# Performance work log

Measured on AMD Instinct MI355X. Metric: run time of the kernel, lower is better.

## Reference

```python
import jax, jax.numpy as jnp
import numpy as np

D_MODEL = 512
D_STATE = 64
L_SEQ = 4096
BATCH = 4


def _make_A(N):
    # HiPPO-LegS style A: A[n,k] = -sqrt(2n+1)sqrt(2k+1) if n>k, -(n+1) if n==k, 0 else (n,k from 1..N)
    idx = np.arange(1, N + 1, dtype=np.float64)
    M = np.sqrt(2 * idx[:, None] + 1) * np.sqrt(2 * idx[None, :] + 1)
    lower = (idx[:, None] > idx[None, :]).astype(np.float64)
    return -(lower * M + np.diag(idx + 1))


def _discretize(A, B, C, step):
    # bilinear (Tustin) transform
    I = np.eye(A.shape[0])
    BL = np.linalg.inv(I - step / 2.0 * A)
    Ab = BL @ (I + step / 2.0 * A)
    Bb = (BL * step) @ B
    return Ab, Bb, C


def setup_inputs() -> dict:
    key = jax.random.key(0)
    rng = np.random.RandomState(0)
    A = _make_A(D_STATE)
    B = rng.randn(D_STATE, 1)
    C = rng.randn(1, D_STATE)
    Ab, Bb, Cb = _discretize(A, B, C, step=1.0 / L_SEQ)
    u = jax.random.normal(key, (BATCH, L_SEQ, D_MODEL), dtype=jnp.float32)
    return {
        "u": u,
        "A_": jnp.asarray(Ab, dtype=jnp.float32),
        "B_": jnp.asarray(Bb, dtype=jnp.float32),
        "C_": jnp.asarray(Cb, dtype=jnp.float32),
    }


def reference(u, A_, B_, C_):
    # u: (B, L, D) -> flatten channels: (BD, L)
    b, L, d = u.shape
    uc = u.transpose(0, 2, 1).reshape(b * d, L)
    N = A_.shape[0]
    b_vec = B_[:, 0]  # (N,)
    c_vec = C_[0]     # (N,)

    def step(x, u_k):
        # x: (BD, N), u_k: (BD,)
        # x_k = A_ @ x_{k-1}^T + B_ @ u_k^T  (expressed batched as x @ A_.T + outer)
        x_new = x @ A_.T + u_k[:, None] * b_vec[None, :]
        y_k = x_new @ c_vec  # (BD,)
        return x_new, y_k

    x0 = jnp.zeros((b * d, N), dtype=u.dtype)
    _, ys = jax.lax.scan(step, x0, uc.T)  # ys: (L, BD)
    y = ys.T.reshape(b, d, L).transpose(0, 2, 1)  # (B, L, D)
    return y
```

## Files before the change

### kernel.cpp

```cpp
#include <hip/hip_runtime.h>

#define L_SEQ   4096
#define D_MODEL 512
#define NSEQ    2048
#define CH      128
#define NC      32

#define OFF_P    0
#define OFF_W1T  4096
#define OFF_WOUT 12288
#define OFF_KLOC 20480
#define OFF_GX   20736

#define BC(v, j) __int_as_float(__builtin_amdgcn_readlane(__float_as_int(v), (j)))

__global__ __launch_bounds__(256) void k_prep(
    const float* __restrict__ A, const float* __restrict__ B,
    const float* __restrict__ C, float* __restrict__ ws) {
  __shared__ float M0[64][68];
  __shared__ float M1[64][68];
  __shared__ float Asv[64][68];
  __shared__ float vrT[128][65];
  __shared__ float Cs[64], Bsh[64];

  const int tid = threadIdx.x;
  if (tid < 64) { Cs[tid] = C[tid]; Bsh[tid] = B[tid]; }
  for (int e = tid; e < 4096; e += 256) {
    const float a = A[e];
    M0[e >> 6][e & 63] = a;
    Asv[e >> 6][e & 63] = a;
  }
  __syncthreads();

  const int iy4 = (tid >> 4) * 4, jx4 = (tid & 15) * 4;
  for (int it = 0; it < 7; ++it) {
    float (*src)[68] = (it & 1) ? M1 : M0;
    float (*dst)[68] = (it & 1) ? M0 : M1;
    float acc[4][4] = {{0.f}};
#pragma unroll 8
    for (int k = 0; k < 64; ++k) {
      const float a0 = src[iy4 + 0][k];
      const float a1 = src[iy4 + 1][k];
      const float a2 = src[iy4 + 2][k];
      const float a3 = src[iy4 + 3][k];
      const float4 b4 = *(const float4*)&src[k][jx4];
      acc[0][0] += a0 * b4.x; acc[0][1] += a0 * b4.y; acc[0][2] += a0 * b4.z; acc[0][3] += a0 * b4.w;
      acc[1][0] += a1 * b4.x; acc[1][1] += a1 * b4.y; acc[1][2] += a1 * b4.z; acc[1][3] += a1 * b4.w;
      acc[2][0] += a2 * b4.x; acc[2][1] += a2 * b4.y; acc[2][2] += a2 * b4.z; acc[2][3] += a2 * b4.w;
      acc[3][0] += a3 * b4.x; acc[3][1] += a3 * b4.y; acc[3][2] += a3 * b4.z; acc[3][3] += a3 * b4.w;
    }
    __syncthreads();
#pragma unroll
    for (int r = 0; r < 4; ++r)
#pragma unroll
      for (int c = 0; c < 4; ++c) dst[iy4 + r][jx4 + c] = acc[r][c];
    __syncthreads();
  }

  float* Pg = ws + OFF_P;
  for (int e = tid; e < 4096; e += 256) Pg[e] = M1[e >> 6][e & 63];

  const int lane = tid & 63, wv = tid >> 6;
  float* Wg = ws + OFF_WOUT;
  float reg[64];
  if (wv == 0) {
#pragma unroll
    for (int j = 0; j < 64; ++j) reg[j] = Asv[lane][j];
    float cur = Bsh[lane];
    vrT[0][lane] = cur;
    for (int m = 1; m < 64; ++m) {
      float nv = 0.f;
#pragma unroll
      for (int j = 0; j < 64; ++j) nv += reg[j] * BC(cur, j);
      cur = nv;
      vrT[m][lane] = cur;
    }
  } else if (wv == 1) {
#pragma unroll
    for (int j = 0; j < 64; ++j) reg[j] = Asv[lane][j];
    const float b0 = Bsh[lane];
    float cur = 0.f;
#pragma unroll
    for (int j = 0; j < 64; ++j) cur += M0[lane][j] * BC(b0, j);
    vrT[64][lane] = cur;
    for (int m = 65; m < 128; ++m) {
      float nv = 0.f;
#pragma unroll
      for (int j = 0; j < 64; ++j) nv += reg[j] * BC(cur, j);
      cur = nv;
      vrT[m][lane] = cur;
    }
  } else if (wv == 2) {
#pragma unroll
    for (int j = 0; j < 64; ++j) reg[j] = Asv[j][lane];
    float cur = Cs[lane];
    for (int m = 1; m <= 64; ++m) {
      float nv = 0.f;
#pragma unroll
      for (int j = 0; j < 64; ++j) nv += BC(cur, j) * reg[j];
      cur = nv;
      Wg[lane * 128 + m - 1] = cur;
    }
  } else {
#pragma unroll
    for (int j = 0; j < 64; ++j) reg[j] = Asv[j][lane];
    const float c0 = Cs[lane];
    float cur = 0.f;
#pragma unroll
    for (int j = 0; j < 64; ++j) cur += BC(c0, j) * M0[j][lane];
    for (int m = 65; m <= 128; ++m) {
      float nv = 0.f;
#pragma unroll
      for (int j = 0; j < 64; ++j) nv += BC(cur, j) * reg[j];
      cur = nv;
      Wg[lane * 128 + m - 1] = cur;
    }
  }
  __syncthreads();

  float* W1Tg = ws + OFF_W1T;
  for (int e = tid; e < 8192; e += 256) {
    const int r = e >> 6, i = e & 63;
    W1Tg[e] = vrT[127 - r][i];
  }

  float* Kz = ws + OFF_KLOC;
  if (tid < 128) {
    float acc = 0.f;
#pragma unroll
    for (int i = 0; i < 64; ++i) acc += Cs[i] * vrT[tid][i];
    Kz[128 + tid] = acc;
  } else {
    Kz[tid - 128] = 0.f;
  }
}

__global__ __launch_bounds__(256) void k_proj(
    const float* __restrict__ u, const float* __restrict__ wsr,
    float* __restrict__ gx) {
  __shared__ float W1s[128][66];
  __shared__ float Us[64][132];

  const int st = blockIdx.x;
  const int c = blockIdx.y;
  const int tid = threadIdx.x;
  const int sgl = st * 128;
  const int bi = sgl >> 9, d0 = sgl & 511;

  const float* W1Tg = wsr + OFF_W1T;
#pragma unroll
  for (int k = 0; k < 32; ++k) {
    const int e = tid + 256 * k;
    W1s[e >> 6][e & 63] = W1Tg[e];
  }

  const float* ub = u + ((size_t)bi * L_SEQ + c * CH) * D_MODEL + d0;
  const int sy4 = (tid >> 3) * 4;
  const int ix8 = (tid & 7) * 8;

  float acc[4][8];
#pragma unroll
  for (int r = 0; r < 4; ++r)
#pragma unroll
    for (int cc = 0; cc < 8; ++cc) acc[r][cc] = 0.f;

  for (int h = 0; h < 2; ++h) {
    __syncthreads();
#pragma unroll
    for (int e8 = 0; e8 < 8; ++e8) {
      const int e = tid + 256 * e8;
      const int rr = e >> 5, s4 = (e & 31) * 4;
      *(float4*)&Us[rr][s4] =
          *(const float4*)(ub + (size_t)(h * 64 + rr) * D_MODEL + s4);
    }
    __syncthreads();
#pragma unroll 4
    for (int rr = 0; rr < 64; ++rr) {
      const int r = h * 64 + rr;
      const float4 a = *(const float4*)&Us[rr][sy4];
      const float4 b0 = *(const float4*)&W1s[r][ix8];
      const float4 b1 = *(const float4*)&W1s[r][ix8 + 4];
      acc[0][0] += a.x * b0.x; acc[0][1] += a.x * b0.y; acc[0][2] += a.x * b0.z; acc[0][3] += a.x * b0.w;
      acc[0][4] += a.x * b1.x; acc[0][5] += a.x * b1.y; acc[0][6] += a.x * b1.z; acc[0][7] += a.x * b1.w;
      acc[1][0] += a.y * b0.x; acc[1][1] += a.y * b0.y; acc[1][2] += a.y * b0.z; acc[1][3] += a.y * b0.w;
      acc[1][4] += a.y * b1.x; acc[1][5] += a.y * b1.y; acc[1][6] += a.y * b1.z; acc[1][7] += a.y * b1.w;
      acc[2][0] += a.z * b0.x; acc[2][1] += a.z * b0.y; acc[2][2] += a.z * b0.z; acc[2][3] += a.z * b0.w;
      acc[2][4] += a.z * b1.x; acc[2][5] += a.z * b1.y; acc[2][6] += a.z * b1.z; acc[2][7] += a.z * b1.w;
      acc[3][0] += a.w * b0.x; acc[3][1] += a.w * b0.y; acc[3][2] += a.w * b0.z; acc[3][3] += a.w * b0.w;
      acc[3][4] += a.w * b1.x; acc[3][5] += a.w * b1.y; acc[3][6] += a.w * b1.z; acc[3][7] += a.w * b1.w;
    }
  }

  float* gb = gx + ((size_t)c * NSEQ + sgl) * 64;
#pragma unroll
  for (int as = 0; as < 4; ++as) {
    float4 v0, v1;
    v0.x = acc[as][0]; v0.y = acc[as][1]; v0.z = acc[as][2]; v0.w = acc[as][3];
    v1.x = acc[as][4]; v1.y = acc[as][5]; v1.z = acc[as][6]; v1.w = acc[as][7];
    float* row = gb + (size_t)(sy4 + as) * 64 + ix8;
    *(float4*)row = v0;
    *(float4*)(row + 4) = v1;
  }
}

__global__ __launch_bounds__(256) void k_scan(
    const float* __restrict__ wsr, float* __restrict__ gx) {
  const int lane = threadIdx.x & 63, wv = threadIdx.x >> 6;
  const int s = blockIdx.x * 4 + wv;

  float p[64];
  {
    const float* pr = wsr + OFF_P + lane * 64;
#pragma unroll
    for (int j = 0; j < 64; j += 4) {
      const float4 v = *(const float4*)(pr + j);
      p[j] = v.x; p[j + 1] = v.y; p[j + 2] = v.z; p[j + 3] = v.w;
    }
  }

  float* gs = gx + (size_t)s * 64 + lane;
  float x = 0.f;
  float g = gs[0];
  for (int c = 0; c < NC; ++c) {
    const float gn = (c + 1 < NC) ? gs[(size_t)(c + 1) * NSEQ * 64] : 0.f;
    gs[(size_t)c * NSEQ * 64] = x;
    float x0 = g, x1 = 0.f;
#pragma unroll
    for (int j = 0; j < 64; j += 2) {
      x0 += p[j] * BC(x, j);
      x1 += p[j + 1] * BC(x, j + 1);
    }
    x = x0 + x1;
    g = gn;
  }
}

__global__ __launch_bounds__(256) void k_localout(
    const float* __restrict__ u, const float* __restrict__ wsr,
    const float* __restrict__ gx, float* __restrict__ out) {
  __shared__ float As[64][68];
  __shared__ float Bs[64][132];

  const int sg = blockIdx.x;
  const int tr = blockIdx.y;
  const int c = tr >> 1, par = tr & 1;
  const int r0 = par * 64;
  const int sgl = sg * 128;
  const int bi = sgl >> 9, d0 = sgl & 511;

  const float* KlocZ = wsr + OFF_KLOC;
  const float* WoutG = wsr + OFF_WOUT;
  const float* ub = u + ((size_t)bi * L_SEQ + c * CH) * D_MODEL + d0;

  const int tid = threadIdx.x;
  const int ty4 = (tid >> 4) * 4;
  const int tx8 = (tid & 15) * 8;

  float acc[4][8];
#pragma unroll
  for (int r = 0; r < 4; ++r)
#pragma unroll
    for (int cc = 0; cc < 8; ++cc) acc[r][cc] = 0.f;

  for (int kt = 0; kt <= par; ++kt) {
    const int k0 = kt * 64;
#pragma unroll
    for (int e8 = 0; e8 < 8; ++e8) {
      const int e = tid + 256 * e8;
      const int kk = e >> 5, s4 = (e & 31) * 4;
      *(float4*)&Bs[kk][s4] = *(const float4*)(ub + (size_t)(k0 + kk) * D_MODEL + s4);
    }
    const int base = 128 + r0 - k0;
#pragma unroll
    for (int e4 = 0; e4 < 16; ++e4) {
      const int e = tid + 256 * e4;
      const int kk = e >> 6, i = e & 63;
      As[kk][i] = KlocZ[base + i - kk];
    }
    __syncthreads();
#pragma unroll 4
    for (int kk = 0; kk < 64; ++kk) {
      const float4 a = *(const float4*)&As[kk][ty4];
      const float4 b0 = *(const float4*)&Bs[kk][tx8];
      const float4 b1 = *(const float4*)&Bs[kk][tx8 + 4];
      acc[0][0] += a.x * b0.x; acc[0][1] += a.x * b0.y; acc[0][2] += a.x * b0.z; acc[0][3] += a.x * b0.w;
      acc[0][4] += a.x * b1.x; acc[0][5] += a.x * b1.y; acc[0][6] += a.x * b1.z; acc[0][7] += a.x * b1.w;
      acc[1][0] += a.y * b0.x; acc[1][1] += a.y * b0.y; acc[1][2] += a.y * b0.z; acc[1][3] += a.y * b0.w;
      acc[1][4] += a.y * b1.x; acc[1][5] += a.y * b1.y; acc[1][6] += a.y * b1.z; acc[1][7] += a.y * b1.w;
      acc[2][0] += a.z * b0.x; acc[2][1] += a.z * b0.y; acc[2][2] += a.z * b0.z; acc[2][3] += a.z * b0.w;
      acc[2][4] += a.z * b1.x; acc[2][5] += a.z * b1.y; acc[2][6] += a.z * b1.z; acc[2][7] += a.z * b1.w;
      acc[3][0] += a.w * b0.x; acc[3][1] += a.w * b0.y; acc[3][2] += a.w * b0.z; acc[3][3] += a.w * b0.w;
      acc[3][4] += a.w * b1.x; acc[3][5] += a.w * b1.y; acc[3][6] += a.w * b1.z; acc[3][7] += a.w * b1.w;
    }
    __syncthreads();
  }

  {
    const float* xc = gx + ((size_t)c * NSEQ + sgl) * 64;
#pragma unroll
    for (int e8 = 0; e8 < 8; ++e8) {
      const int e = tid + 256 * e8;
      const int sl = e >> 4, i4 = (e & 15) * 4;
      const float4 v = *(const float4*)(xc + (size_t)sl * 64 + i4);
      Bs[i4 + 0][sl] = v.x;
      Bs[i4 + 1][sl] = v.y;
      Bs[i4 + 2][sl] = v.z;
      Bs[i4 + 3][sl] = v.w;
    }
#pragma unroll
    for (int e4 = 0; e4 < 16; ++e4) {
      const int e = tid + 256 * e4;
      const int i_ = e >> 6, r = e & 63;
      As[i_][r] = WoutG[i_ * 128 + r0 + r];
    }
    __syncthreads();
#pragma unroll 4
    for (int kk = 0; kk < 64; ++kk) {
      const float4 a = *(const float4*)&As[kk][ty4];
      const float4 b0 = *(const float4*)&Bs[kk][tx8];
      const float4 b1 = *(const float4*)&Bs[kk][tx8 + 4];
      acc[0][0] += a.x * b0.x; acc[0][1] += a.x * b0.y; acc[0][2] += a.x * b0.z; acc[0][3] += a.x * b0.w;
      acc[0][4] += a.x * b1.x; acc[0][5] += a.x * b1.y; acc[0][6] += a.x * b1.z; acc[0][7] += a.x * b1.w;
      acc[1][0] += a.y * b0.x; acc[1][1] += a.y * b0.y; acc[1][2] += a.y * b0.z; acc[1][3] += a.y * b0.w;
      acc[1][4] += a.y * b1.x; acc[1][5] += a.y * b1.y; acc[1][6] += a.y * b1.z; acc[1][7] += a.y * b1.w;
      acc[2][0] += a.z * b0.x; acc[2][1] += a.z * b0.y; acc[2][2] += a.z * b0.z; acc[2][3] += a.z * b0.w;
      acc[2][4] += a.z * b1.x; acc[2][5] += a.z * b1.y; acc[2][6] += a.z * b1.z; acc[2][7] += a.z * b1.w;
      acc[3][0] += a.w * b0.x; acc[3][1] += a.w * b0.y; acc[3][2] += a.w * b0.z; acc[3][3] += a.w * b0.w;
      acc[3][4] += a.w * b1.x; acc[3][5] += a.w * b1.y; acc[3][6] += a.w * b1.z; acc[3][7] += a.w * b1.w;
    }
  }

  float* ob = out + ((size_t)bi * L_SEQ + c * CH + r0) * D_MODEL + d0;
#pragma unroll
  for (int r = 0; r < 4; ++r) {
    float4 v0, v1;
    v0.x = acc[r][0]; v0.y = acc[r][1]; v0.z = acc[r][2]; v0.w = acc[r][3];
    v1.x = acc[r][4]; v1.y = acc[r][5]; v1.z = acc[r][6]; v1.w = acc[r][7];
    float* row = ob + (size_t)(ty4 + r) * D_MODEL + tx8;
    *(float4*)row = v0;
    *(float4*)(row + 4) = v1;
  }
}

extern "C" void kernel_launch(void* const* d_in, const int* in_sizes, int n_in,
                              void* d_out, int out_size, void* d_ws,
                              size_t ws_size, hipStream_t stream) {
  const float* u = (const float*)d_in[0];
  const float* A = (const float*)d_in[1];
  const float* B = (const float*)d_in[2];
  const float* C = (const float*)d_in[3];
  float* out = (float*)d_out;
  float* ws = (float*)d_ws;
  float* gx = ws + OFF_GX;

  k_prep<<<1, 256, 0, stream>>>(A, B, C, ws);
  k_proj<<<dim3(16, 32), 256, 0, stream>>>(u, ws, gx);
  k_scan<<<512, 256, 0, stream>>>(ws, gx);
  k_localout<<<dim3(16, 64), 256, 0, stream>>>(u, ws, gx, out);
}
```

Measured before the change: 209.3 us.

## Transpose gx state layout and retile all four kernels around it

The chunk-state buffer gx changes from sequence-major to state-index-major layout, so k_proj writes and k_localout reads contiguous sequences. k_scan now runs 1024-thread blocks that stage the state through LDS to transpose it, and double-buffers the next chunk's input. k_localout handles a whole 128-row chunk per block over 64 sequences, reads kernel taps and Wout straight from global memory, and skips the upper-triangle zero block for the first half. k_prep keeps transposed copies of its matrices so the squaring loop can use vectorised LDS loads. These touch several unrelated costs at once, and they add extra barriers in the scan loop and uncached global loads in the inner loops.

```diff
diff --git a/kernel.cpp b/kernel.cpp
--- a/kernel.cpp
+++ b/kernel.cpp
@@ -14,106 +14,143 @@
 
 #define BC(v, j) __int_as_float(__builtin_amdgcn_readlane(__float_as_int(v), (j)))
 
+#define FMAC84(acc, a0, a1, b)                                                \
+  acc[0][0]+=a0.x*b.x; acc[0][1]+=a0.x*b.y; acc[0][2]+=a0.x*b.z; acc[0][3]+=a0.x*b.w; \
+  acc[1][0]+=a0.y*b.x; acc[1][1]+=a0.y*b.y; acc[1][2]+=a0.y*b.z; acc[1][3]+=a0.y*b.w; \
+  acc[2][0]+=a0.z*b.x; acc[2][1]+=a0.z*b.y; acc[2][2]+=a0.z*b.z; acc[2][3]+=a0.z*b.w; \
+  acc[3][0]+=a0.w*b.x; acc[3][1]+=a0.w*b.y; acc[3][2]+=a0.w*b.z; acc[3][3]+=a0.w*b.w; \
+  acc[4][0]+=a1.x*b.x; acc[4][1]+=a1.x*b.y; acc[4][2]+=a1.x*b.z; acc[4][3]+=a1.x*b.w; \
+  acc[5][0]+=a1.y*b.x; acc[5][1]+=a1.y*b.y; acc[5][2]+=a1.y*b.z; acc[5][3]+=a1.y*b.w; \
+  acc[6][0]+=a1.z*b.x; acc[6][1]+=a1.z*b.y; acc[6][2]+=a1.z*b.z; acc[6][3]+=a1.z*b.w; \
+  acc[7][0]+=a1.w*b.x; acc[7][1]+=a1.w*b.y; acc[7][2]+=a1.w*b.z; acc[7][3]+=a1.w*b.w;
+
 __global__ __launch_bounds__(256) void k_prep(
     const float* __restrict__ A, const float* __restrict__ B,
     const float* __restrict__ C, float* __restrict__ ws) {
-  __shared__ float M0[64][68];
-  __shared__ float M1[64][68];
-  __shared__ float Asv[64][68];
+  __shared__ float M0[64][68], M0T[64][68], M1[64][68], M1T[64][68];
+  __shared__ float Asv[64][68], AsvT[64][68];
   __shared__ float vrT[128][65];
   __shared__ float Cs[64], Bsh[64];
 
   const int tid = threadIdx.x;
   if (tid < 64) { Cs[tid] = C[tid]; Bsh[tid] = B[tid]; }
   for (int e = tid; e < 4096; e += 256) {
+    const int i = e >> 6, j = e & 63;
     const float a = A[e];
-    M0[e >> 6][e & 63] = a;
-    Asv[e >> 6][e & 63] = a;
-  }
-  __syncthreads();
-
-  const int iy4 = (tid >> 4) * 4, jx4 = (tid & 15) * 4;
+    M0[i][j] = a; M0T[j][i] = a;
+    Asv[i][j] = a; AsvT[j][i] = a;
+  }
+  __syncthreads();
+
+  const int rt = (tid >> 4) * 8;
+  const int ct = (tid & 15) * 4;
   for (int it = 0; it < 7; ++it) {
-    float (*src)[68] = (it & 1) ? M1 : M0;
-    float (*dst)[68] = (it & 1) ? M0 : M1;
-    float acc[4][4] = {{0.f}};
+    if (tid < 128) {
+      float (*src)[68]  = (it & 1) ? M1 : M0;
+      float (*srcT)[68] = (it & 1) ? M1T : M0T;
+      float (*dst)[68]  = (it & 1) ? M0 : M1;
+      float (*dstT)[68] = (it & 1) ? M0T : M1T;
+      float acc[8][4] = {{0.f}};
 #pragma unroll 8
-    for (int k = 0; k < 64; ++k) {
-      const float a0 = src[iy4 + 0][k];
-      const float a1 = src[iy4 + 1][k];
-      const float a2 = src[iy4 + 2][k];
-      const float a3 = src[iy4 + 3][k];
-      const float4 b4 = *(const float4*)&src[k][jx4];
-      acc[0][0] += a0 * b4.x; acc[0][1] += a0 * b4.y; acc[0][2] += a0 * b4.z; acc[0][3] += a0 * b4.w;
-      acc[1][0] += a1 * b4.x; acc[1][1] += a1 * b4.y; acc[1][2] += a1 * b4.z; acc[1][3] += a1 * b4.w;
-      acc[2][0] += a2 * b4.x; acc[2][1] += a2 * b4.y; acc[2][2] += a2 * b4.z; acc[2][3] += a2 * b4.w;
-      acc[3][0] += a3 * b4.x; acc[3][1] += a3 * b4.y; acc[3][2] += a3 * b4.z; acc[3][3] += a3 * b4.w;
-    }
-    __syncthreads();
-#pragma unroll
-    for (int r = 0; r < 4; ++r)
-#pragma unroll
-      for (int c = 0; c < 4; ++c) dst[iy4 + r][jx4 + c] = acc[r][c];
-    __syncthreads();
-  }
-
-  float* Pg = ws + OFF_P;
-  for (int e = tid; e < 4096; e += 256) Pg[e] = M1[e >> 6][e & 63];
+      for (int k = 0; k < 64; ++k) {
+        const float4 a0 = *(const float4*)&srcT[k][rt];
+        const float4 a1 = *(const float4*)&srcT[k][rt + 4];
+        const float4 b  = *(const float4*)&src[k][ct];
+        FMAC84(acc, a0, a1, b);
+      }
+#pragma unroll
+      for (int j = 0; j < 8; ++j) {
+        float4 v; v.x = acc[j][0]; v.y = acc[j][1]; v.z = acc[j][2]; v.w = acc[j][3];
+        *(float4*)&dst[rt + j][ct] = v;
+      }
+#pragma unroll
+      for (int cc = 0; cc < 4; ++cc) {
+        float4 v0, v1;
+        v0.x = acc[0][cc]; v0.y = acc[1][cc]; v0.z = acc[2][cc]; v0.w = acc[3][cc];
+        v1.x = acc[4][cc]; v1.y = acc[5][cc]; v1.z = acc[6][cc]; v1.w = acc[7][cc];
+        *(float4*)&dstT[ct + cc][rt] = v0;
+        *(float4*)&dstT[ct + cc][rt + 4] = v1;
+      }
+    }
+    __syncthreads();
+  }
 
   const int lane = tid & 63, wv = tid >> 6;
   float* Wg = ws + OFF_WOUT;
-  float reg[64];
-  if (wv == 0) {
-#pragma unroll
-    for (int j = 0; j < 64; ++j) reg[j] = Asv[lane][j];
-    float cur = Bsh[lane];
-    vrT[0][lane] = cur;
-    for (int m = 1; m < 64; ++m) {
-      float nv = 0.f;
-#pragma unroll
-      for (int j = 0; j < 64; ++j) nv += reg[j] * BC(cur, j);
-      cur = nv;
-      vrT[m][lane] = cur;
-    }
-  } else if (wv == 1) {
-#pragma unroll
-    for (int j = 0; j < 64; ++j) reg[j] = Asv[lane][j];
-    const float b0 = Bsh[lane];
-    float cur = 0.f;
-#pragma unroll
-    for (int j = 0; j < 64; ++j) cur += M0[lane][j] * BC(b0, j);
-    vrT[64][lane] = cur;
-    for (int m = 65; m < 128; ++m) {
-      float nv = 0.f;
-#pragma unroll
-      for (int j = 0; j < 64; ++j) nv += reg[j] * BC(cur, j);
-      cur = nv;
-      vrT[m][lane] = cur;
-    }
-  } else if (wv == 2) {
-#pragma unroll
-    for (int j = 0; j < 64; ++j) reg[j] = Asv[j][lane];
-    float cur = Cs[lane];
-    for (int m = 1; m <= 64; ++m) {
-      float nv = 0.f;
-#pragma unroll
-      for (int j = 0; j < 64; ++j) nv += BC(cur, j) * reg[j];
-      cur = nv;
-      Wg[lane * 128 + m - 1] = cur;
-    }
-  } else {
-#pragma unroll
-    for (int j = 0; j < 64; ++j) reg[j] = Asv[j][lane];
-    const float c0 = Cs[lane];
-    float cur = 0.f;
-#pragma unroll
-    for (int j = 0; j < 64; ++j) cur += BC(c0, j) * M0[j][lane];
-    for (int m = 65; m <= 128; ++m) {
-      float nv = 0.f;
-#pragma unroll
-      for (int j = 0; j < 64; ++j) nv += BC(cur, j) * reg[j];
-      cur = nv;
-      Wg[lane * 128 + m - 1] = cur;
+  {
+    float reg[64];
+    if (wv == 0) {
+#pragma unroll
+      for (int j4 = 0; j4 < 16; ++j4) {
+        const float4 v = *(const float4*)&Asv[lane][j4 * 4];
+        reg[j4*4] = v.x; reg[j4*4+1] = v.y; reg[j4*4+2] = v.z; reg[j4*4+3] = v.w;
+      }
+      float cur = Bsh[lane];
+      vrT[0][lane] = cur;
+      for (int m = 1; m < 64; ++m) {
+        float nv = 0.f;
+#pragma unroll
+        for (int j = 0; j < 64; ++j) nv += reg[j] * BC(cur, j);
+        cur = nv;
+        vrT[m][lane] = cur;
+      }
+    } else if (wv == 1) {
+#pragma unroll
+      for (int j4 = 0; j4 < 16; ++j4) {
+        const float4 v = *(const float4*)&Asv[lane][j4 * 4];
+        reg[j4*4] = v.x; reg[j4*4+1] = v.y; reg[j4*4+2] = v.z; reg[j4*4+3] = v.w;
+      }
+      const float b0 = Bsh[lane];
+      float cur = 0.f;
+#pragma unroll
+      for (int j4 = 0; j4 < 16; ++j4) {
+        const float4 v = *(const float4*)&M0[lane][j4 * 4];
+        cur += v.x * BC(b0, j4*4) + v.y * BC(b0, j4*4+1) +
+               v.z * BC(b0, j4*4+2) + v.w * BC(b0, j4*4+3);
+      }
+      vrT[64][lane] = cur;
+      for (int m = 65; m < 128; ++m) {
+        float nv = 0.f;
+#pragma unroll
+        for (int j = 0; j < 64; ++j) nv += reg[j] * BC(cur, j);
+        cur = nv;
+        vrT[m][lane] = cur;
+      }
+    } else if (wv == 2) {
+#pragma unroll
+      for (int j4 = 0; j4 < 16; ++j4) {
+        const float4 v = *(const float4*)&AsvT[lane][j4 * 4];
+        reg[j4*4] = v.x; reg[j4*4+1] = v.y; reg[j4*4+2] = v.z; reg[j4*4+3] = v.w;
+      }
+      float cur = Cs[lane];
+      for (int m = 1; m <= 64; ++m) {
+        float nv = 0.f;
+#pragma unroll
+        for (int j = 0; j < 64; ++j) nv += reg[j] * BC(cur, j);
+        cur = nv;
+        Wg[lane * 128 + m - 1] = cur;
+      }
+    } else {
+#pragma unroll
+      for (int j4 = 0; j4 < 16; ++j4) {
+        const float4 v = *(const float4*)&AsvT[lane][j4 * 4];
+        reg[j4*4] = v.x; reg[j4*4+1] = v.y; reg[j4*4+2] = v.z; reg[j4*4+3] = v.w;
+      }
+      const float c0 = Cs[lane];
+      float cur = 0.f;
+#pragma unroll
+      for (int j4 = 0; j4 < 16; ++j4) {
+        const float4 v = *(const float4*)&M0T[lane][j4 * 4];
+        cur += v.x * BC(c0, j4*4) + v.y * BC(c0, j4*4+1) +
+               v.z * BC(c0, j4*4+2) + v.w * BC(c0, j4*4+3);
+      }
+      for (int m = 65; m <= 128; ++m) {
+        float nv = 0.f;
+#pragma unroll
+        for (int j = 0; j < 64; ++j) nv += reg[j] * BC(cur, j);
+        cur = nv;
+        Wg[lane * 128 + m - 1] = cur;
+      }
     }
   }
   __syncthreads();
@@ -123,7 +160,6 @@
     const int r = e >> 6, i = e & 63;
     W1Tg[e] = vrT[127 - r][i];
   }
-
   float* Kz = ws + OFF_KLOC;
   if (tid < 128) {
     float acc = 0.f;
@@ -133,97 +169,82 @@
   } else {
     Kz[tid - 128] = 0.f;
   }
-}
-
-__global__ __launch_bounds__(256) void k_proj(
+  float* Pg = ws + OFF_P;
+  for (int e = tid; e < 4096; e += 256) Pg[e] = M1[e >> 6][e & 63];
+}
+
+__global__ __launch_bounds__(128) void k_proj(
     const float* __restrict__ u, const float* __restrict__ wsr,
     float* __restrict__ gx) {
-  __shared__ float W1s[128][66];
-  __shared__ float Us[64][132];
+  __shared__ float Us[64][64];
 
   const int st = blockIdx.x;
-  const int c = blockIdx.y;
+  const int c  = blockIdx.y;
   const int tid = threadIdx.x;
-  const int sgl = st * 128;
-  const int bi = sgl >> 9, d0 = sgl & 511;
-
+  const int s0 = st * 64;
+  const int bi = s0 >> 9, d0 = s0 & 511;
   const float* W1Tg = wsr + OFF_W1T;
-#pragma unroll
-  for (int k = 0; k < 32; ++k) {
-    const int e = tid + 256 * k;
-    W1s[e >> 6][e & 63] = W1Tg[e];
-  }
-
   const float* ub = u + ((size_t)bi * L_SEQ + c * CH) * D_MODEL + d0;
-  const int sy4 = (tid >> 3) * 4;
-  const int ix8 = (tid & 7) * 8;
-
-  float acc[4][8];
-#pragma unroll
-  for (int r = 0; r < 4; ++r)
-#pragma unroll
-    for (int cc = 0; cc < 8; ++cc) acc[r][cc] = 0.f;
-
+  const int ig = tid >> 4;
+  const int sg = tid & 15;
+
+  float acc[8][4] = {{0.f}};
   for (int h = 0; h < 2; ++h) {
     __syncthreads();
 #pragma unroll
-    for (int e8 = 0; e8 < 8; ++e8) {
-      const int e = tid + 256 * e8;
-      const int rr = e >> 5, s4 = (e & 31) * 4;
-      *(float4*)&Us[rr][s4] =
+    for (int n = 0; n < 8; ++n) {
+      const int e = tid + 128 * n;
+      const int rr = e >> 4, s4 = (e & 15) * 4;
+      *(((float4*)Us) + e) =
           *(const float4*)(ub + (size_t)(h * 64 + rr) * D_MODEL + s4);
     }
     __syncthreads();
 #pragma unroll 4
     for (int rr = 0; rr < 64; ++rr) {
-      const int r = h * 64 + rr;
-      const float4 a = *(const float4*)&Us[rr][sy4];
-      const float4 b0 = *(const float4*)&W1s[r][ix8];
-      const float4 b1 = *(const float4*)&W1s[r][ix8 + 4];
-      acc[0][0] += a.x * b0.x; acc[0][1] += a.x * b0.y; acc[0][2] += a.x * b0.z; acc[0][3] += a.x * b0.w;
-      acc[0][4] += a.x * b1.x; acc[0][5] += a.x * b1.y; acc[0][6] += a.x * b1.z; acc[0][7] += a.x * b1.w;
-      acc[1][0] += a.y * b0.x; acc[1][1] += a.y * b0.y; acc[1][2] += a.y * b0.z; acc[1][3] += a.y * b0.w;
-      acc[1][4] += a.y * b1.x; acc[1][5] += a.y * b1.y; acc[1][6] += a.y * b1.z; acc[1][7] += a.y * b1.w;
-      acc[2][0] += a.z * b0.x; acc[2][1] += a.z * b0.y; acc[2][2] += a.z * b0.z; acc[2][3] += a.z * b0.w;
-      acc[2][4] += a.z * b1.x; acc[2][5] += a.z * b1.y; acc[2][6] += a.z * b1.z; acc[2][7] += a.z * b1.w;
-      acc[3][0] += a.w * b0.x; acc[3][1] += a.w * b0.y; acc[3][2] += a.w * b0.z; acc[3][3] += a.w * b0.w;
-      acc[3][4] += a.w * b1.x; acc[3][5] += a.w * b1.y; acc[3][6] += a.w * b1.z; acc[3][7] += a.w * b1.w;
-    }
-  }
-
-  float* gb = gx + ((size_t)c * NSEQ + sgl) * 64;
-#pragma unroll
-  for (int as = 0; as < 4; ++as) {
-    float4 v0, v1;
-    v0.x = acc[as][0]; v0.y = acc[as][1]; v0.z = acc[as][2]; v0.w = acc[as][3];
-    v1.x = acc[as][4]; v1.y = acc[as][5]; v1.z = acc[as][6]; v1.w = acc[as][7];
-    float* row = gb + (size_t)(sy4 + as) * 64 + ix8;
-    *(float4*)row = v0;
-    *(float4*)(row + 4) = v1;
-  }
-}
-
-__global__ __launch_bounds__(256) void k_scan(
+      const float* wr = W1Tg + (size_t)(h * 64 + rr) * 64 + ig * 8;
+      const float4 a0 = *(const float4*)wr;
+      const float4 a1 = *(const float4*)(wr + 4);
+      const float4 b  = *(const float4*)&Us[rr][sg * 4];
+      FMAC84(acc, a0, a1, b);
+    }
+  }
+
+  float* gb = gx + (size_t)c * 64 * NSEQ + s0 + sg * 4;
+#pragma unroll
+  for (int j = 0; j < 8; ++j) {
+    float4 v; v.x = acc[j][0]; v.y = acc[j][1]; v.z = acc[j][2]; v.w = acc[j][3];
+    *(float4*)(gb + (size_t)(ig * 8 + j) * NSEQ) = v;
+  }
+}
+
+__global__ __launch_bounds__(1024) void k_scan(
     const float* __restrict__ wsr, float* __restrict__ gx) {
-  const int lane = threadIdx.x & 63, wv = threadIdx.x >> 6;
-  const int s = blockIdx.x * 4 + wv;
+  __shared__ float gbuf[2][64][17];
+  __shared__ float xbuf[64][17];
+  const int tid = threadIdx.x;
+  const int lane = tid & 63, wv = tid >> 6;
+  const int s0 = blockIdx.x * 16;
+  const int ci = tid >> 4, cj = tid & 15;
 
   float p[64];
-  {
-    const float* pr = wsr + OFF_P + lane * 64;
-#pragma unroll
-    for (int j = 0; j < 64; j += 4) {
-      const float4 v = *(const float4*)(pr + j);
-      p[j] = v.x; p[j + 1] = v.y; p[j + 2] = v.z; p[j + 3] = v.w;
-    }
-  }
-
-  float* gs = gx + (size_t)s * 64 + lane;
+#pragma unroll
+  for (int j4 = 0; j4 < 16; ++j4) {
+    const float4 v = *(const float4*)(wsr + OFF_P + lane * 64 + j4 * 4);
+    p[j4*4] = v.x; p[j4*4+1] = v.y; p[j4*4+2] = v.z; p[j4*4+3] = v.w;
+  }
+
+  gbuf[0][ci][cj] = gx[(size_t)ci * NSEQ + s0 + cj];
+  __syncthreads();
+
   float x = 0.f;
-  float g = gs[0];
   for (int c = 0; c < NC; ++c) {
-    const float gn = (c + 1 < NC) ? gs[(size_t)(c + 1) * NSEQ * 64] : 0.f;
-    gs[(size_t)c * NSEQ * 64] = x;
+    const int buf = c & 1;
+    if (c + 1 < NC)
+      gbuf[buf ^ 1][ci][cj] = gx[(size_t)((c + 1) * 64 + ci) * NSEQ + s0 + cj];
+    xbuf[lane][wv] = x;
+    __syncthreads();
+    gx[(size_t)(c * 64 + ci) * NSEQ + s0 + cj] = xbuf[ci][cj];
+    const float g = gbuf[buf][lane][wv];
     float x0 = g, x1 = 0.f;
 #pragma unroll
     for (int j = 0; j < 64; j += 2) {
@@ -231,114 +252,91 @@
       x1 += p[j + 1] * BC(x, j + 1);
     }
     x = x0 + x1;
-    g = gn;
+    __syncthreads();
   }
 }
 
 __global__ __launch_bounds__(256) void k_localout(
     const float* __restrict__ u, const float* __restrict__ wsr,
     const float* __restrict__ gx, float* __restrict__ out) {
-  __shared__ float As[64][68];
-  __shared__ float Bs[64][132];
-
-  const int sg = blockIdx.x;
-  const int tr = blockIdx.y;
-  const int c = tr >> 1, par = tr & 1;
-  const int r0 = par * 64;
-  const int sgl = sg * 128;
-  const int bi = sgl >> 9, d0 = sgl & 511;
-
+  __shared__ float Bs[64][64];
+
+  const int st = blockIdx.x;
+  const int c  = blockIdx.y;
+  const int tid = threadIdx.x;
+  const int s0 = st * 64;
+  const int bi = s0 >> 9, d0 = s0 & 511;
+  const int rg = tid >> 4;
+  const int sq = tid & 15;
   const float* KlocZ = wsr + OFF_KLOC;
   const float* WoutG = wsr + OFF_WOUT;
   const float* ub = u + ((size_t)bi * L_SEQ + c * CH) * D_MODEL + d0;
 
-  const int tid = threadIdx.x;
-  const int ty4 = (tid >> 4) * 4;
-  const int tx8 = (tid & 15) * 8;
-
-  float acc[4][8];
-#pragma unroll
-  for (int r = 0; r < 4; ++r)
-#pragma unroll
-    for (int cc = 0; cc < 8; ++cc) acc[r][cc] = 0.f;
-
-  for (int kt = 0; kt <= par; ++kt) {
-    const int k0 = kt * 64;
-#pragma unroll
-    for (int e8 = 0; e8 < 8; ++e8) {
-      const int e = tid + 256 * e8;
-      const int kk = e >> 5, s4 = (e & 31) * 4;
-      *(float4*)&Bs[kk][s4] = *(const float4*)(ub + (size_t)(k0 + kk) * D_MODEL + s4);
-    }
-    const int base = 128 + r0 - k0;
-#pragma unroll
-    for (int e4 = 0; e4 < 16; ++e4) {
-      const int e = tid + 256 * e4;
-      const int kk = e >> 6, i = e & 63;
-      As[kk][i] = KlocZ[base + i - kk];
-    }
-    __syncthreads();
+  float acc[8][4] = {{0.f}};
+
+#pragma unroll
+  for (int n = 0; n < 4; ++n) {
+    const int e = tid + 256 * n;
+    *(((float4*)Bs) + e) =
+        *(const float4*)(ub + (size_t)(e >> 4) * D_MODEL + (e & 15) * 4);
+  }
+  __syncthreads();
+  {
+    const float* k0p = KlocZ + 128 + rg * 8;
 #pragma unroll 4
     for (int kk = 0; kk < 64; ++kk) {
-      const float4 a = *(const float4*)&As[kk][ty4];
-      const float4 b0 = *(const float4*)&Bs[kk][tx8];
-      const float4 b1 = *(const float4*)&Bs[kk][tx8 + 4];
-      acc[0][0] += a.x * b0.x; acc[0][1] += a.x * b0.y; acc[0][2] += a.x * b0.z; acc[0][3] += a.x * b0.w;
-      acc[0][4] += a.x * b1.x; acc[0][5] += a.x * b1.y; acc[0][6] += a.x * b1.z; acc[0][7] += a.x * b1.w;
-      acc[1][0] += a.y * b0.x; acc[1][1] += a.y * b0.y; acc[1][2] += a.y * b0.z; acc[1][3] += a.y * b0.w;
-      acc[1][4] += a.y * b1.x; acc[1][5] += a.y * b1.y; acc[1][6] += a.y * b1.z; acc[1][7] += a.y * b1.w;
-      acc[2][0] += a.z * b0.x; acc[2][1] += a.z * b0.y; acc[2][2] += a.z * b0.z; acc[2][3] += a.z * b0.w;
-      acc[2][4] += a.z * b1.x; acc[2][5] += a.z * b1.y; acc[2][6] += a.z * b1.z; acc[2][7] += a.z * b1.w;
-      acc[3][0] += a.w * b0.x; acc[3][1] += a.w * b0.y; acc[3][2] += a.w * b0.z; acc[3][3] += a.w * b0.w;
-      acc[3][4] += a.w * b1.x; acc[3][5] += a.w * b1.y; acc[3][6] += a.w * b1.z; acc[3][7] += a.w * b1.w;
-    }
-    __syncthreads();
-  }
-
-  {
-    const float* xc = gx + ((size_t)c * NSEQ + sgl) * 64;
-#pragma unroll
-    for (int e8 = 0; e8 < 8; ++e8) {
-      const int e = tid + 256 * e8;
-      const int sl = e >> 4, i4 = (e & 15) * 4;
-      const float4 v = *(const float4*)(xc + (size_t)sl * 64 + i4);
-      Bs[i4 + 0][sl] = v.x;
-      Bs[i4 + 1][sl] = v.y;
-      Bs[i4 + 2][sl] = v.z;
-      Bs[i4 + 3][sl] = v.w;
-    }
-#pragma unroll
-    for (int e4 = 0; e4 < 16; ++e4) {
-      const int e = tid + 256 * e4;
-      const int i_ = e >> 6, r = e & 63;
-      As[i_][r] = WoutG[i_ * 128 + r0 + r];
-    }
-    __syncthreads();
+      float4 a0, a1;
+      __builtin_memcpy(&a0, k0p - kk, 16);
+      __builtin_memcpy(&a1, k0p - kk + 4, 16);
+      const float4 b = *(const float4*)&Bs[kk][sq * 4];
+      FMAC84(acc, a0, a1, b);
+    }
+  }
+  __syncthreads();
+
+#pragma unroll
+  for (int n = 0; n < 4; ++n) {
+    const int e = tid + 256 * n;
+    *(((float4*)Bs) + e) =
+        *(const float4*)(ub + (size_t)(64 + (e >> 4)) * D_MODEL + (e & 15) * 4);
+  }
+  __syncthreads();
+  if (rg >= 8) {
+    const float* k0p = KlocZ + 64 + rg * 8;
 #pragma unroll 4
     for (int kk = 0; kk < 64; ++kk) {
-      const float4 a = *(const float4*)&As[kk][ty4];
-      const float4 b0 = *(const float4*)&Bs[kk][tx8];
-      const float4 b1 = *(const float4*)&Bs[kk][tx8 + 4];
-      acc[0][0] += a.x * b0.x; acc[0][1] += a.x * b0.y; acc[0][2] += a.x * b0.z; acc[0][3] += a.x * b0.w;
-      acc[0][4] += a.x * b1.x; acc[0][5] += a.x * b1.y; acc[0][6] += a.x * b1.z; acc[0][7] += a.x * b1.w;
-      acc[1][0] += a.y * b0.x; acc[1][1] += a.y * b0.y; acc[1][2] += a.y * b0.z; acc[1][3] += a.y * b0.w;
-      acc[1][4] += a.y * b1.x; acc[1][5] += a.y * b1.y; acc[1][6] += a.y * b1.z; acc[1][7] += a.y * b1.w;
-      acc[2][0] += a.z * b0.x; acc[2][1] += a.z * b0.y; acc[2][2] += a.z * b0.z; acc[2][3] += a.z * b0.w;
-      acc[2][4] += a.z * b1.x; acc[2][5] += a.z * b1.y; acc[2][6] += a.z * b1.z; acc[2][7] += a.z * b1.w;
-      acc[3][0] += a.w * b0.x; acc[3][1] += a.w * b0.y; acc[3][2] += a.w * b0.z; acc[3][3] += a.w * b0.w;
-      acc[3][4] += a.w * b1.x; acc[3][5] += a.w * b1.y; acc[3][6] += a.w * b1.z; acc[3][7] += a.w * b1.w;
-    }
-  }
-
-  float* ob = out + ((size_t)bi * L_SEQ + c * CH + r0) * D_MODEL + d0;
-#pragma unroll
-  for (int r = 0; r < 4; ++r) {
-    float4 v0, v1;
-    v0.x = acc[r][0]; v0.y = acc[r][1]; v0.z = acc[r][2]; v0.w = acc[r][3];
-    v1.x = acc[r][4]; v1.y = acc[r][5]; v1.z = acc[r][6]; v1.w = acc[r][7];
-    float* row = ob + (size_t)(ty4 + r) * D_MODEL + tx8;
-    *(float4*)row = v0;
-    *(float4*)(row + 4) = v1;
+      float4 a0, a1;
+      __builtin_memcpy(&a0, k0p - kk, 16);
+      __builtin_memcpy(&a1, k0p - kk + 4, 16);
+      const float4 b = *(const float4*)&Bs[kk][sq * 4];
+      FMAC84(acc, a0, a1, b);
+    }
+  }
+  __syncthreads();
+
+#pragma unroll
+  for (int n = 0; n < 4; ++n) {
+    const int e = tid + 256 * n;
+    *(((float4*)Bs) + e) = *(const float4*)(
+        gx + (size_t)(c * 64 + (e >> 4)) * NSEQ + s0 + (e & 15) * 4);
+  }
+  __syncthreads();
+  {
+#pragma unroll 4
+    for (int kk = 0; kk < 64; ++kk) {
+      const float* wp = WoutG + kk * 128 + rg * 8;
+      const float4 a0 = *(const float4*)wp;
+      const float4 a1 = *(const float4*)(wp + 4);
+      const float4 b = *(const float4*)&Bs[kk][sq * 4];
+      FMAC84(acc, a0, a1, b);
+    }
+  }
+
+  float* ob = out + ((size_t)bi * L_SEQ + c * CH) * D_MODEL + d0 + sq * 4;
+#pragma unroll
+  for (int j = 0; j < 8; ++j) {
+    float4 v; v.x = acc[j][0]; v.y = acc[j][1]; v.z = acc[j][2]; v.w = acc[j][3];
+    *(float4*)(ob + (size_t)(rg * 8 + j) * D_MODEL) = v;
   }
 }
 
@@ -354,7 +352,7 @@
   float* gx = ws + OFF_GX;
 
   k_prep<<<1, 256, 0, stream>>>(A, B, C, ws);
-  k_proj<<<dim3(16, 32), 256, 0, stream>>>(u, ws, gx);
-  k_scan<<<512, 256, 0, stream>>>(ws, gx);
-  k_localout<<<dim3(16, 64), 256, 0, stream>>>(u, ws, gx, out);
-}
+  k_proj<<<dim3(32, 32), 128, 0, stream>>>(u, ws, gx);
+  k_scan<<<128, 1024, 0, stream>>>(ws, gx);
+  k_localout<<<dim3(32, 32), 256, 0, stream>>>(u, ws, gx, out);
+}
```

New measurement: 247.8 us. 18.4% more time.
